# Optimization experiments

Measured on AMD Instinct MI355X. Metric: run time of the kernel, lower is better.

## Reference

```python
import jax, jax.numpy as jnp
import numpy as np

C, PE, L, HEADS = 256, 64, 6, 4
N_GRAPHS, S = 2048, 64            # uniform graphs of S nodes -> dense batch is a reshape
N = N_GRAPHS * S                  # 131072 nodes
E = N * 4                         # 524288 edges
BN_EPS = 1e-5


def _bn(h, g, b):
    # BatchNorm1d, training-mode statistics (biased variance), affine
    m = h.mean(0)
    v = h.var(0)
    return (h - m) / jnp.sqrt(v + BN_EPS) * g + b


def setup_inputs() -> dict:
    key = jax.random.key(0)
    ks = iter(jax.random.split(key, 64))
    def rn(shape, scale=0.05):
        return jax.random.normal(next(ks), shape, dtype=jnp.float32) * scale
    x = jax.random.randint(next(ks), (N, 1), 0, 28)
    pe = jax.random.normal(next(ks), (N, 20), dtype=jnp.float32)
    epg = E // N_GRAPHS
    base = (jnp.arange(E) // epg) * S          # edges stay within their graph
    src = base + jax.random.randint(next(ks), (E,), 0, S)
    dst = base + jax.random.randint(next(ks), (E,), 0, S)
    edge_index = jnp.stack([src, dst])
    edge_attr = jax.random.randint(next(ks), (E,), 0, 4)
    batch = jnp.arange(N) // S
    return dict(
        x=x, pe=pe, edge_index=edge_index, edge_attr=edge_attr, batch=batch,
        node_emb=rn((28, C - PE), 1.0), pe_lin_w=rn((20, PE)), pe_lin_b=jnp.zeros(PE),
        pe_norm_g=jnp.ones(20), pe_norm_b=jnp.zeros(20),
        edge_emb=rn((4, C), 1.0),
        conv_w1=rn((L, C, C)), conv_b1=jnp.zeros((L, C)),
        conv_w2=rn((L, C, C)), conv_b2=jnp.zeros((L, C)),
        attn_in_w=rn((L, C, 3 * C)), attn_in_b=jnp.zeros((L, 3 * C)),
        attn_out_w=rn((L, C, C)), attn_out_b=jnp.zeros((L, C)),
        bn1_g=jnp.ones((L, C)), bn1_b=jnp.zeros((L, C)),
        bn2_g=jnp.ones((L, C)), bn2_b=jnp.zeros((L, C)),
        bn3_g=jnp.ones((L, C)), bn3_b=jnp.zeros((L, C)),
        mlp_w1=rn((L, C, 2 * C)), mlp_b1=jnp.zeros((L, 2 * C)),
        mlp_w2=rn((L, 2 * C, C)), mlp_b2=jnp.zeros((L, C)),
        head_w1=rn((C, C // 2)), head_b1=jnp.zeros(C // 2),
        head_w2=rn((C // 2, C // 4)), head_b2=jnp.zeros(C // 4),
        head_w3=rn((C // 4, 1)), head_b3=jnp.zeros(1),
    )


def reference(x, pe, edge_index, edge_attr, batch, node_emb, pe_lin_w, pe_lin_b,
              pe_norm_g, pe_norm_b, edge_emb, conv_w1, conv_b1, conv_w2, conv_b2,
              attn_in_w, attn_in_b, attn_out_w, attn_out_b,
              bn1_g, bn1_b, bn2_g, bn2_b, bn3_g, bn3_b,
              mlp_w1, mlp_b1, mlp_w2, mlp_b2,
              head_w1, head_b1, head_w2, head_b2, head_w3, head_b3):
    x_pe = _bn(pe, pe_norm_g, pe_norm_b)
    h = jnp.concatenate([node_emb[x[:, 0]], x_pe @ pe_lin_w + pe_lin_b], axis=1)  # [N, C]
    ea = edge_emb[edge_attr]                                                      # [E, C]
    src, dst = edge_index[0], edge_index[1]
    d = C // HEADS
    scale = 1.0 / jnp.sqrt(jnp.float32(d))
    for l in range(L):
        # --- local GINEConv: nn((1+eps)*x_i + sum_j relu(x_j + e_ij)), eps=0 ---
        msg = jax.nn.relu(h[src] + ea)                          # gather + add + relu
        aggr = jax.ops.segment_sum(msg, dst, num_segments=N)    # scatter-add
        z = h + aggr
        hl = jax.nn.relu(z @ conv_w1[l] + conv_b1[l]) @ conv_w2[l] + conv_b2[l]
        hl = _bn(hl + h, bn1_g[l], bn1_b[l])                    # residual + norm1
        # --- global multihead attention on dense batch [G, S, C] ---
        hd = h.reshape(N_GRAPHS, S, C)
        qkv = hd @ attn_in_w[l] + attn_in_b[l]
        q, k, v = jnp.split(qkv, 3, axis=-1)
        q = q.reshape(N_GRAPHS, S, HEADS, d).transpose(0, 2, 1, 3)
        k = k.reshape(N_GRAPHS, S, HEADS, d).transpose(0, 2, 1, 3)
        v = v.reshape(N_GRAPHS, S, HEADS, d).transpose(0, 2, 1, 3)
        a = jax.nn.softmax(jnp.einsum('ghqd,ghkd->ghqk', q, k) * scale, axis=-1)
        o = jnp.einsum('ghqk,ghkd->ghqd', a, v).transpose(0, 2, 1, 3).reshape(N_GRAPHS, S, C)
        o = (o @ attn_out_w[l] + attn_out_b[l]).reshape(N, C)
        ha = _bn(o + h, bn2_g[l], bn2_b[l])                     # residual + norm2
        # --- combine + FFN ---
        out = hl + ha
        ff = jax.nn.relu(out @ mlp_w1[l] + mlp_b1[l]) @ mlp_w2[l] + mlp_b2[l]
        h = _bn(out + ff, bn3_g[l], bn3_b[l])                   # residual + norm3
    pooled = jax.ops.segment_sum(h, batch, num_segments=N_GRAPHS)  # global_add_pool -> [G, C]
    t = jax.nn.relu(pooled @ head_w1 + head_b1)
    t = jax.nn.relu(t @ head_w2 + head_b2)
    return t @ head_w3 + head_b3                                   # [G, 1]
```

## Files before the change

### kernel.cpp

```cpp
#include <hip/hip_runtime.h>

#define N_NODES 131072
#define N_EDGES 524288
#define CCH 256
#define N_GRAPHS_ 2048
#define SEQ 64
#define LAYERS 6

typedef unsigned short US;
typedef __attribute__((ext_vector_type(8))) short v8s;
typedef __attribute__((ext_vector_type(8))) unsigned short v8us;
typedef __attribute__((ext_vector_type(4))) float v4f;

__device__ __forceinline__ float b2f(US u) { return __uint_as_float(((unsigned)u) << 16); }
__device__ __forceinline__ US f2b(float f) {
    unsigned u = __float_as_uint(f);
    return (US)((u + 0x7fff + ((u >> 16) & 1)) >> 16);
}
__device__ __forceinline__ void gload16(const US* g, US* l) {
    __builtin_amdgcn_global_load_lds(
        (const __attribute__((address_space(1))) unsigned int*)g,
        (__attribute__((address_space(3))) unsigned int*)l, 16, 0, 0);
}

__device__ float g_stats[512];
__device__ float g_aff1[512];
__device__ float g_aff2[512];
__device__ float g_aff3[512];
__device__ float g_pe[40];
__device__ float g_peaff[40];
__device__ US    g_wt[6 * 655360];
__device__ int   g_csr[N_EDGES];
__device__ int   g_off[N_GRAPHS_ * 65];

__global__ __launch_bounds__(256) void wt_k(const float* __restrict__ cw1, const float* __restrict__ cw2,
                                            const float* __restrict__ aiw, const float* __restrict__ aow,
                                            const float* __restrict__ mw1, const float* __restrict__ mw2) {
    __shared__ float t[64][65];
    int b = blockIdx.x;
    int l = b / 160, r = b % 160;
    const float* src; int ldw, ldk, ctiles; size_t doff;
    if (r < 16)      { src = cw1 + (size_t)l * 65536;  ldw = 256; ldk = 256; ctiles = 4;  doff = 0;      }
    else if (r < 32) { src = cw2 + (size_t)l * 65536;  ldw = 256; ldk = 256; ctiles = 4;  doff = 65536;  r -= 16; }
    else if (r < 80) { src = aiw + (size_t)l * 196608; ldw = 768; ldk = 256; ctiles = 12; doff = 131072; r -= 32; }
    else if (r < 96) { src = aow + (size_t)l * 65536;  ldw = 256; ldk = 256; ctiles = 4;  doff = 327680; r -= 80; }
    else if (r < 128){ src = mw1 + (size_t)l * 131072; ldw = 512; ldk = 256; ctiles = 8;  doff = 393216; r -= 96; }
    else             { src = mw2 + (size_t)l * 131072; ldw = 256; ldk = 512; ctiles = 4;  doff = 524288; r -= 128; }
    int kt = r / ctiles, ct = r % ctiles;
    int k0 = kt * 64, c0 = ct * 64;
    US* dst = g_wt + (size_t)l * 655360 + doff;
    int tid = threadIdx.x;
    int rr = tid >> 4, c4 = (tid & 15) * 4;
    #pragma unroll
    for (int j = 0; j < 4; j++) {
        float4 v = *(const float4*)(src + (size_t)(k0 + rr + j * 16) * ldw + c0 + c4);
        t[rr + j * 16][c4 + 0] = v.x; t[rr + j * 16][c4 + 1] = v.y;
        t[rr + j * 16][c4 + 2] = v.z; t[rr + j * 16][c4 + 3] = v.w;
    }
    __syncthreads();
    #pragma unroll
    for (int j = 0; j < 4; j++) {
        int crow = rr + j * 16;
        ushort4 o;
        o.x = f2b(t[c4 + 0][crow]); o.y = f2b(t[c4 + 1][crow]);
        o.z = f2b(t[c4 + 2][crow]); o.w = f2b(t[c4 + 3][crow]);
        *(ushort4*)(dst + (size_t)(c0 + crow) * ldk + k0 + c4) = o;
    }
}

__global__ __launch_bounds__(256) void csr_k(const int* __restrict__ ei,
                                             const int* __restrict__ attr) {
    __shared__ int deg[64], off[65];
    int g = blockIdx.x, tid = threadIdx.x;
    if (tid < 64) deg[tid] = 0;
    __syncthreads();
    int e = g * 256 + tid;
    int d = ei[N_EDGES + e] - g * 64;
    int slot = atomicAdd(&deg[d], 1);
    __syncthreads();
    if (tid == 0) {
        off[0] = 0;
        for (int i = 0; i < 64; i++) off[i + 1] = off[i] + deg[i];
    }
    __syncthreads();
    g_csr[g * 256 + off[d] + slot] = (ei[e] - g * 64) | (attr[e] << 6);
    if (tid < 65) g_off[g * 65 + tid] = off[tid];
}

__global__ __launch_bounds__(256) void pe_part_k(const float* __restrict__ pe) {
    __shared__ float red[240], red2[240];
    int b = blockIdx.x, tid = threadIdx.x;
    float s = 0.f, s2 = 0.f;
    if (tid < 240) {
        int ch = tid % 20, sub = tid / 20;
        size_t r0 = (size_t)b * 512;
        for (int r = sub; r < 512; r += 12) {
            float v = pe[(r0 + r) * 20 + ch];
            s += v; s2 += v * v;
        }
        red[tid] = s; red2[tid] = s2;
    }
    __syncthreads();
    if (tid < 20) {
        float ts = 0.f, ts2 = 0.f;
        #pragma unroll
        for (int sub = 0; sub < 12; sub++) { ts += red[sub * 20 + tid]; ts2 += red2[sub * 20 + tid]; }
        atomicAdd(&g_pe[tid], ts);
        atomicAdd(&g_pe[20 + tid], ts2);
    }
}

__global__ __launch_bounds__(64) void pe_fin_k(const float* __restrict__ g,
                                               const float* __restrict__ b) {
    int t = threadIdx.x;
    if (t < 20) {
        float mean = g_pe[t] / (float)N_NODES;
        float var  = g_pe[20 + t] / (float)N_NODES - mean * mean;
        float a = g[t] * rsqrtf(var + 1e-5f);
        g_peaff[t] = a;
        g_peaff[20 + t] = b[t] - mean * a;
        g_pe[t] = 0.f;
        g_pe[20 + t] = 0.f;
    }
}

__global__ __launch_bounds__(256) void embed_k(const int* __restrict__ x,
                                               const float* __restrict__ pe,
                                               const float* __restrict__ node_emb,
                                               const float* __restrict__ plw,
                                               const float* __restrict__ plb,
                                               US* __restrict__ h) {
    int n = blockIdx.x;
    int tid = threadIdx.x;
    int xi = x[n];
    float v;
    if (tid < 192) {
        v = node_emb[xi * 192 + tid];
    } else {
        int j = tid - 192;
        float s = plb[j];
        #pragma unroll
        for (int k = 0; k < 20; k++) {
            float p = pe[(size_t)n * 20 + k] * g_peaff[k] + g_peaff[20 + k];
            s += p * plw[k * 64 + j];
        }
        v = s;
    }
    h[(size_t)n * CCH + tid] = f2b(v);
}

__global__ __launch_bounds__(256) void apply_k(US* __restrict__ h) {
    size_t idx = (size_t)blockIdx.x * 256 + threadIdx.x;
    size_t stride = (size_t)gridDim.x * 256;
    for (; idx < (size_t)N_NODES * CCH / 8; idx += stride) {
        size_t i = idx * 8;
        int c = (int)(i & 255);
        v8us a = *(const v8us*)(h + i);
        v8us o;
        #pragma unroll
        for (int j = 0; j < 8; j++)
            o[j] = f2b(b2f(a[j]) * g_aff3[c + j] + g_aff3[CCH + c + j]);
        *(v8us*)(h + i) = o;
    }
}

__global__ __launch_bounds__(256) void aggr_z_k(const US* __restrict__ h,
                                                const float* __restrict__ eemb,
                                                US* __restrict__ z) {
    __shared__ US ht[64 * 264];
    __shared__ float em[4 * 260];
    __shared__ int off[65], ce[256];
    int g = blockIdx.x, tid = threadIdx.x;
    for (int v = tid; v < 2048; v += 256) {
        int row = v >> 5, seg = (v & 31) * 8;
        *(v8us*)&ht[row * 264 + seg] = *(const v8us*)(h + (size_t)(g * 64 + row) * 256 + seg);
    }
    for (int i = tid; i < 1024; i += 256)
        em[(i >> 8) * 260 + (i & 255)] = eemb[(i >> 8) * 256 + (i & 255)];
    ce[tid] = g_csr[g * 256 + tid];
    if (tid < 65) off[tid] = g_off[g * 65 + tid];
    __syncthreads();

    int dst = tid >> 2, cq = (tid & 3) * 4;
    float acc[64];
    #pragma unroll
    for (int i = 0; i < 64; i++) acc[i] = 0.f;
    int e1 = off[dst + 1];
    for (int e = off[dst]; e < e1; e++) {
        int val = ce[e];
        int src = val & 63, a = (val >> 6) & 3;
        #pragma unroll
        for (int i = 0; i < 16; i++) {
            int c = cq + i * 16;
            ushort4 hv = *(ushort4*)&ht[src * 264 + c];
            float4 ev = *(float4*)&em[a * 260 + c];
            acc[i * 4 + 0] += fmaxf(b2f(hv.x) + ev.x, 0.f);
            acc[i * 4 + 1] += fmaxf(b2f(hv.y) + ev.y, 0.f);
            acc[i * 4 + 2] += fmaxf(b2f(hv.z) + ev.z, 0.f);
            acc[i * 4 + 3] += fmaxf(b2f(hv.w) + ev.w, 0.f);
        }
    }
    US* zp = z + (size_t)(g * 64 + dst) * 256;
    #pragma unroll
    for (int i = 0; i < 16; i++) {
        int c = cq + i * 16;
        ushort4 hv = *(ushort4*)&ht[dst * 264 + c];
        ushort4 o;
        o.x = f2b(b2f(hv.x) + acc[i * 4 + 0]);
        o.y = f2b(b2f(hv.y) + acc[i * 4 + 1]);
        o.z = f2b(b2f(hv.z) + acc[i * 4 + 2]);
        o.w = f2b(b2f(hv.w) + acc[i * 4 + 3]);
        *(ushort4*)(zp + c) = o;
    }
}

template<int NG, bool STATS>
__global__ __launch_bounds__(256, 4) void gemm_mfma_k(const US* __restrict__ A,
                                                      size_t woff, int ldk,
                                                      int w0, int w1, int w2, int w3,
                                                      const float* __restrict__ bias,
                                                      const US* __restrict__ res,
                                                      US* __restrict__ Y, int mode) {
    const US* __restrict__ Wt = g_wt + woff;
    __shared__ __align__(16) char smem[8192 + 2 * NG * 4096];
    US* As0 = (US*)smem;
    US* As1 = As0 + 2048;
    US* Bs0 = (US*)(smem + 8192);
    US* Bs1 = Bs0 + NG * 2048;
    float* Es = (float*)smem;
    const int NW = NG * 64 + 4;

    int tid = threadIdx.x;
    int bid = blockIdx.x;
    int swz = (bid & 7) * ((int)gridDim.x >> 3) + (bid >> 3);
    size_t row0 = (size_t)swz * 64;
    int w = tid >> 6, l = tid & 63;
    int li = l & 15, hi = l >> 4;
    int sl = hi ^ ((li >> 1) & 3);
    int sr = l >> 2, ss = l & 3;

    int a_off = (w * 16 + li) * 32 + sl * 8;

    v4f acc[NG * 4];
    #pragma unroll
    for (int t = 0; t < NG * 4; t++) acc[t] = (v4f){0.f, 0.f, 0.f, 0.f};

    int ar = w * 16 + sr;
    int akg = (ss ^ ((ar >> 1) & 3)) * 8;
    const US* asrc = A + (row0 + ar) * 256 + akg;

    auto stage = [&](int kc, US* Asb, US* Bsb) {
        int k0 = kc * 32;
        gload16(asrc + k0, Asb + w * 512);
        #pragma unroll
        for (int j = 0; j < NG; j++) {
            int cu = (j * 4 + w) * 16 + sr;
            int grp = cu >> 6;
            int wb = (grp == 0) ? w0 : (grp == 1) ? w1 : (grp == 2) ? w2 : w3;
            int kg = (ss ^ ((cu >> 1) & 3)) * 8;
            gload16(Wt + (size_t)(wb + (cu & 63)) * ldk + k0 + kg,
                    Bsb + (j * 4 + w) * 512);
        }
    };

    stage(0, As0, Bs0);
    __syncthreads();
    for (int kc = 0; kc < 8; kc++) {
        US* Asc = (kc & 1) ? As1 : As0;
        US* Bsc = (kc & 1) ? Bs1 : Bs0;
        if (kc < 7) stage(kc + 1, (kc & 1) ? As0 : As1, (kc & 1) ? Bs0 : Bs1);
        v8s a0 = *(v8s*)(Asc + a_off);
        #pragma unroll
        for (int t = 0; t < NG * 4; t++) {
            v8s bf = *(v8s*)(Bsc + (t * 16 + li) * 32 + sl * 8);
            acc[t] = __builtin_amdgcn_mfma_f32_16x16x32_bf16(a0, bf, acc[t], 0, 0, 0);
        }
        __syncthreads();
    }

    int er_f = tid >> 3;
    int lcb = (tid & 7) * 8;
    float csum = 0.f, csum2 = 0.f;
    #pragma unroll
    for (int p = 0; p < 2; p++) {
        if ((w >> 1) == p) {
            int er0 = (w & 1) * 16 + hi * 4;
            #pragma unroll
            for (int t = 0; t < NG * 4; t++) {
                int grp = t >> 2;
                int wb = (grp == 0) ? w0 : (grp == 1) ? w1 : (grp == 2) ? w2 : w3;
                float bv = bias ? bias[wb + (t & 3) * 16 + li] : 0.f;
                #pragma unroll
                for (int r = 0; r < 4; r++) {
                    float v = acc[t][r] + bv;
                    if (mode == 1) v = fmaxf(v, 0.f);
                    Es[(er0 + r) * NW + t * 16 + li] = v;
                }
            }
        }
        __syncthreads();
        size_t gr = row0 + p * 32 + er_f;
        #pragma unroll
        for (int s = 0; s < NG; s++) {
            int c = s * 64 + lcb;
            float vs[8];
            #pragma unroll
            for (int j = 0; j < 8; j++) vs[j] = Es[er_f * NW + c + j];
            if (mode == 2) {
                v8us rv = *(const v8us*)(res + gr * 256 + c);
                #pragma unroll
                for (int j = 0; j < 8; j++) vs[j] += b2f(rv[j]);
            }
            v8us yv;
            #pragma unroll
            for (int j = 0; j < 8; j++) yv[j] = f2b(vs[j]);
            *(v8us*)(Y + gr * 256 + c) = yv;
            if constexpr (STATS) {
                #pragma unroll
                for (int j = 0; j < 8; j++) Es[er_f * NW + c + j] = vs[j];
            }
        }
        if constexpr (STATS) {
            __syncthreads();
            if (tid < NG * 64) {
                float s1 = 0.f, s2 = 0.f;
                #pragma unroll 8
                for (int r2 = 0; r2 < 32; r2++) {
                    float vv = Es[r2 * NW + tid];
                    s1 += vv; s2 += vv * vv;
                }
                csum += s1; csum2 += s2;
            }
        }
        __syncthreads();
    }
    if constexpr (STATS) {
        if (tid < NG * 64) {
            atomicAdd(&g_stats[tid], csum);
            atomicAdd(&g_stats[CCH + tid], csum2);
        }
    }
}

template<int NH>
__global__ __launch_bounds__(256, 2) void mlp_fused_k(const US* __restrict__ A,
                                                      size_t woff1, const float* __restrict__ bias1,
                                                      size_t woff2, int ldk2,
                                                      const float* __restrict__ bias2,
                                                      const US* __restrict__ res,
                                                      US* __restrict__ Y) {
    const US* __restrict__ W1t = g_wt + woff1;
    const US* __restrict__ W2t = g_wt + woff2;
    __shared__ __align__(16) char smem[73728];
    US* As0 = (US*)smem;
    US* As1 = (US*)(smem + 4096);
    US* Bs0 = (US*)(smem + 8192);
    US* Bs1 = (US*)(smem + 24576);
    float* Es = (float*)smem;
    US* Ts = (US*)(smem + 40960);

    int tid = threadIdx.x;
    int bid = blockIdx.x;
    int swz = (bid & 7) * ((int)gridDim.x >> 3) + (bid >> 3);
    size_t row0 = (size_t)swz * 64;
    int w = tid >> 6, l = tid & 63;
    int li = l & 15, hi = l >> 4;
    int sl = hi ^ ((li >> 1) & 3);
    int sr = l >> 2, ss = l & 3;

    int a_off = (w * 16 + li) * 32 + sl * 8;

    v4f accY[16];
    #pragma unroll
    for (int t = 0; t < 16; t++) accY[t] = (v4f){0.f, 0.f, 0.f, 0.f};

    int ar = w * 16 + sr;
    int akg = (ss ^ ((ar >> 1) & 3)) * 8;
    const US* asrc = A + (row0 + ar) * 256 + akg;

    #pragma unroll
    for (int q = 0; q < NH; q++) {
        v4f accT[16];
        #pragma unroll
        for (int t = 0; t < 16; t++) accT[t] = (v4f){0.f, 0.f, 0.f, 0.f};

        auto stageA = [&](int kc, US* Asb, US* Bsb) {
            int k0 = kc * 32;
            gload16(asrc + k0, Asb + w * 512);
            #pragma unroll
            for (int j = 0; j < 4; j++) {
                int cu = (j * 4 + w) * 16 + sr;
                int kg = (ss ^ ((cu >> 1) & 3)) * 8;
                gload16(W1t + (size_t)(q * 256 + cu) * 256 + k0 + kg,
                        Bsb + (j * 4 + w) * 512);
            }
        };
        stageA(0, As0, Bs0);
        __syncthreads();
        for (int kc = 0; kc < 8; kc++) {
            US* Asc = (kc & 1) ? As1 : As0;
            US* Bsc = (kc & 1) ? Bs1 : Bs0;
            if (kc < 7) stageA(kc + 1, (kc & 1) ? As0 : As1, (kc & 1) ? Bs0 : Bs1);
            v8s a0 = *(v8s*)(Asc + a_off);
            #pragma unroll
            for (int t = 0; t < 16; t++) {
                v8s bf = *(v8s*)(Bsc + (t * 16 + li) * 32 + sl * 8);
                accT[t] = __builtin_amdgcn_mfma_f32_16x16x32_bf16(a0, bf, accT[t], 0, 0, 0);
            }
            __syncthreads();
        }
        #pragma unroll
        for (int p = 0; p < 2; p++) {
            if ((w >> 1) == p) {
                int er0 = (w & 1) * 16 + hi * 4;
                #pragma unroll
                for (int t = 0; t < 16; t++) {
                    float bv = bias1[q * 256 + t * 16 + li];
                    #pragma unroll
                    for (int r = 0; r < 4; r++)
                        Es[(er0 + r) * 260 + t * 16 + li] = fmaxf(accT[t][r] + bv, 0.f);
                }
            }
            __syncthreads();
            {
                int er = tid >> 3, lcb = (tid & 7) * 8;
                int rowL = p * 32 + er;
                int rsw = (rowL >> 1) & 3;
                #pragma unroll
                for (int s = 0; s < 4; s++) {
                    int col = s * 64 + lcb;
                    v8us tv;
                    #pragma unroll
                    for (int j = 0; j < 8; j++) tv[j] = f2b(Es[er * 260 + col + j]);
                    int chunk = col >> 5, slot = ((col >> 3) & 3) ^ rsw;
                    *(v8us*)&Ts[chunk * 2048 + rowL * 32 + slot * 8] = tv;
                }
            }
            __syncthreads();
        }
        auto stageB = [&](int kc, US* Bsb) {
            int k0 = q * 256 + kc * 32;
            #pragma unroll
            for (int j = 0; j < 4; j++) {
                int cu = (j * 4 + w) * 16 + sr;
                int kg = (ss ^ ((cu >> 1) & 3)) * 8;
                gload16(W2t + (size_t)cu * ldk2 + k0 + kg, Bsb + (j * 4 + w) * 512);
            }
        };
        stageB(0, Bs0);
        __syncthreads();
        for (int kc = 0; kc < 8; kc++) {
            US* Bsc = (kc & 1) ? Bs1 : Bs0;
            if (kc < 7) stageB(kc + 1, (kc & 1) ? Bs0 : Bs1);
            v8s a0 = *(v8s*)(Ts + kc * 2048 + a_off);
            #pragma unroll
            for (int t = 0; t < 16; t++) {
                v8s bf = *(v8s*)(Bsc + (t * 16 + li) * 32 + sl * 8);
                accY[t] = __builtin_amdgcn_mfma_f32_16x16x32_bf16(a0, bf, accY[t], 0, 0, 0);
            }
            __syncthreads();
        }
    }

    int er_f = tid >> 3;
    int lcb = (tid & 7) * 8;
    float csum = 0.f, csum2 = 0.f;
    #pragma unroll
    for (int p = 0; p < 2; p++) {
        if ((w >> 1) == p) {
            int er0 = (w & 1) * 16 + hi * 4;
            #pragma unroll
            for (int t = 0; t < 16; t++) {
                float bv = bias2[t * 16 + li];
                #pragma unroll
                for (int r = 0; r < 4; r++)
                    Es[(er0 + r) * 260 + t * 16 + li] = accY[t][r] + bv;
            }
        }
        __syncthreads();
        size_t gr = row0 + p * 32 + er_f;
        #pragma unroll
        for (int s = 0; s < 4; s++) {
            int c = s * 64 + lcb;
            float vs[8];
            #pragma unroll
            for (int j = 0; j < 8; j++) vs[j] = Es[er_f * 260 + c + j];
            v8us rv = *(const v8us*)(res + gr * 256 + c);
            #pragma unroll
            for (int j = 0; j < 8; j++) vs[j] += b2f(rv[j]);
            v8us yv;
            #pragma unroll
            for (int j = 0; j < 8; j++) yv[j] = f2b(vs[j]);
            *(v8us*)(Y + gr * 256 + c) = yv;
            #pragma unroll
            for (int j = 0; j < 8; j++) Es[er_f * 260 + c + j] = vs[j];
        }
        __syncthreads();
        {
            float s1 = 0.f, s2 = 0.f;
            #pragma unroll 8
            for (int r2 = 0; r2 < 32; r2++) {
                float vv = Es[r2 * 260 + tid];
                s1 += vv; s2 += vv * vv;
            }
            csum += s1; csum2 += s2;
        }
        __syncthreads();
    }
    atomicAdd(&g_stats[tid], csum);
    atomicAdd(&g_stats[CCH + tid], csum2);
}

__global__ __launch_bounds__(64) void attn_k(US* __restrict__ qb,
                                             const US* __restrict__ kb,
                                             const US* __restrict__ vb) {
    __shared__ __align__(16) US Ps[64 * 72];
    __shared__ __align__(16) US Vt[64 * 72];
    int g = blockIdx.x, l = threadIdx.x;
    int coff = blockIdx.y * 64;
    int li = l & 15, hi8 = (l >> 4) * 8, hi4 = (l >> 4) * 4;
    size_t rb = (size_t)g * 64 * 256;

    {
        v8us vv[8];
        #pragma unroll
        for (int jv = 0; jv < 8; jv++)
            vv[jv] = *(const v8us*)(vb + rb + l * 256 + coff + jv * 8);
        #pragma unroll
        for (int jv = 0; jv < 8; jv++)
            #pragma unroll
            for (int e = 0; e < 8; e++)
                Vt[(jv * 8 + e) * 72 + l] = vv[jv][e];
    }

    v8s Qf[4][2], Kf[4][2];
    #pragma unroll
    for (int t = 0; t < 4; t++)
        #pragma unroll
        for (int ds = 0; ds < 2; ds++) {
            Qf[t][ds] = *(const v8s*)(qb + rb + (t * 16 + li) * 256 + coff + ds * 32 + hi8);
            Kf[t][ds] = *(const v8s*)(kb + rb + (t * 16 + li) * 256 + coff + ds * 32 + hi8);
        }

    v4f S[4][4];
    #pragma unroll
    for (int qt = 0; qt < 4; qt++)
        #pragma unroll
        for (int kt = 0; kt < 4; kt++) {
            v4f a = (v4f){0.f, 0.f, 0.f, 0.f};
            a = __builtin_amdgcn_mfma_f32_16x16x32_bf16(Qf[qt][0], Kf[kt][0], a, 0, 0, 0);
            a = __builtin_amdgcn_mfma_f32_16x16x32_bf16(Qf[qt][1], Kf[kt][1], a, 0, 0, 0);
            S[qt][kt] = a;
        }

    #pragma unroll
    for (int qt = 0; qt < 4; qt++)
        #pragma unroll
        for (int r = 0; r < 4; r++) {
            float mx = -1e30f;
            #pragma unroll
            for (int kt = 0; kt < 4; kt++) {
                S[qt][kt][r] *= 0.125f;
                mx = fmaxf(mx, S[qt][kt][r]);
            }
            mx = fmaxf(mx, __shfl_xor(mx, 1));
            mx = fmaxf(mx, __shfl_xor(mx, 2));
            mx = fmaxf(mx, __shfl_xor(mx, 4));
            mx = fmaxf(mx, __shfl_xor(mx, 8));
            float sum = 0.f;
            #pragma unroll
            for (int kt = 0; kt < 4; kt++) {
                float e = __expf(S[qt][kt][r] - mx);
                S[qt][kt][r] = e;
                sum += e;
            }
            sum += __shfl_xor(sum, 1);
            sum += __shfl_xor(sum, 2);
            sum += __shfl_xor(sum, 4);
            sum += __shfl_xor(sum, 8);
            float inv = 1.f / sum;
            #pragma unroll
            for (int kt = 0; kt < 4; kt++)
                Ps[(qt * 16 + hi4 + r) * 72 + kt * 16 + li] = f2b(S[qt][kt][r] * inv);
        }

    v4f O[4][4];
    #pragma unroll
    for (int qt = 0; qt < 4; qt++)
        #pragma unroll
        for (int jt = 0; jt < 4; jt++) O[qt][jt] = (v4f){0.f, 0.f, 0.f, 0.f};
    #pragma unroll
    for (int ks = 0; ks < 2; ks++) {
        v8s Pf[4], Vf[4];
        #pragma unroll
        for (int qt = 0; qt < 4; qt++)
            Pf[qt] = *(v8s*)&Ps[(qt * 16 + li) * 72 + ks * 32 + hi8];
        #pragma unroll
        for (int jt = 0; jt < 4; jt++)
            Vf[jt] = *(v8s*)&Vt[(jt * 16 + li) * 72 + ks * 32 + hi8];
        #pragma unroll
        for (int qt = 0; qt < 4; qt++)
            #pragma unroll
            for (int jt = 0; jt < 4; jt++)
                O[qt][jt] = __builtin_amdgcn_mfma_f32_16x16x32_bf16(Pf[qt], Vf[jt], O[qt][jt], 0, 0, 0);
    }

    __syncthreads();
    #pragma unroll
    for (int qt = 0; qt < 4; qt++)
        #pragma unroll
        for (int jt = 0; jt < 4; jt++)
            #pragma unroll
            for (int r = 0; r < 4; r++)
                Ps[(qt * 16 + hi4 + r) * 72 + jt * 16 + li] = f2b(O[qt][jt][r]);
    __syncthreads();
    US* ob = qb + rb + l * 256 + coff;
    #pragma unroll
    for (int jv = 0; jv < 8; jv++)
        *(v8us*)(ob + jv * 8) = *(v8us*)&Ps[l * 72 + jv * 8];
}

__global__ __launch_bounds__(256) void affine_k(const float* __restrict__ g,
                                                const float* __restrict__ b, int sel) {
    int c = threadIdx.x;
    float mean = g_stats[c] / (float)N_NODES;
    float var  = g_stats[CCH + c] / (float)N_NODES - mean * mean;
    float a = g[c] * rsqrtf(var + 1e-5f);
    float* dst = (sel == 0) ? g_aff1 : (sel == 1) ? g_aff2 : g_aff3;
    dst[c] = a;
    dst[CCH + c] = b[c] - mean * a;
    g_stats[c] = 0.f;
    g_stats[CCH + c] = 0.f;
}

__global__ __launch_bounds__(256) void combine_k(const US* __restrict__ y1,
                                                 const US* __restrict__ y2,
                                                 US* __restrict__ out) {
    size_t idx = (size_t)blockIdx.x * 256 + threadIdx.x;
    size_t stride = (size_t)gridDim.x * 256;
    for (; idx < (size_t)N_NODES * CCH / 8; idx += stride) {
        size_t i = idx * 8;
        int c = (int)(i & 255);
        v8us a = *(const v8us*)(y1 + i);
        v8us b = *(const v8us*)(y2 + i);
        v8us o;
        #pragma unroll
        for (int j = 0; j < 8; j++) {
            float v = b2f(a[j]) * g_aff1[c + j] + g_aff1[CCH + c + j] +
                      b2f(b[j]) * g_aff2[c + j] + g_aff2[CCH + c + j];
            o[j] = f2b(v);
        }
        *(v8us*)(out + i) = o;
    }
}

__global__ __launch_bounds__(256) void pool_k(const US* __restrict__ h,
                                              float* __restrict__ pooled) {
    int g = blockIdx.x, c = threadIdx.x;
    float s = 0.f;
    for (int ss = 0; ss < SEQ; ss++) s += b2f(h[((size_t)g * SEQ + ss) * CCH + c]);
    pooled[(size_t)g * CCH + c] = g_aff3[c] * s + 64.f * g_aff3[CCH + c];
}

__global__ __launch_bounds__(128) void head_k(const float* __restrict__ pooled,
                                              const float* __restrict__ w1, const float* __restrict__ b1,
                                              const float* __restrict__ w2, const float* __restrict__ b2,
                                              const float* __restrict__ w3, const float* __restrict__ b3,
                                              float* __restrict__ outp) {
    __shared__ float p[256], t1[128], t2[64];
    int g = blockIdx.x, tid = threadIdx.x;
    p[tid] = pooled[(size_t)g * CCH + tid];
    p[tid + 128] = pooled[(size_t)g * CCH + 128 + tid];
    __syncthreads();
    float s = b1[tid];
    for (int k = 0; k < 256; k++) s += p[k] * w1[k * 128 + tid];
    t1[tid] = fmaxf(s, 0.f);
    __syncthreads();
    if (tid < 64) {
        float s2 = b2[tid];
        for (int k = 0; k < 128; k++) s2 += t1[k] * w2[k * 64 + tid];
        t2[tid] = fmaxf(s2, 0.f);
    }
    __syncthreads();
    if (tid == 0) {
        float s3 = b3[0];
        for (int k = 0; k < 64; k++) s3 += t2[k] * w3[k];
        outp[g] = s3;
    }
}

extern "C" void kernel_launch(void* const* d_in, const int* in_sizes, int n_in,
                              void* d_out, int out_size, void* d_ws, size_t ws_size,
                              hipStream_t stream) {
    const int*   x         = (const int*)  d_in[0];
    const float* pe        = (const float*)d_in[1];
    const int*   ei        = (const int*)  d_in[2];
    const int*   eattr     = (const int*)  d_in[3];
    const float* node_emb  = (const float*)d_in[5];
    const float* pe_lin_w  = (const float*)d_in[6];
    const float* pe_lin_b  = (const float*)d_in[7];
    const float* pe_norm_g = (const float*)d_in[8];
    const float* pe_norm_b = (const float*)d_in[9];
    const float* edge_emb  = (const float*)d_in[10];
    const float* conv_w1   = (const float*)d_in[11];
    const float* conv_b1   = (const float*)d_in[12];
    const float* conv_w2   = (const float*)d_in[13];
    const float* conv_b2   = (const float*)d_in[14];
    const float* attn_in_w = (const float*)d_in[15];
    const float* attn_in_b = (const float*)d_in[16];
    const float* attn_out_w= (const float*)d_in[17];
    const float* attn_out_b= (const float*)d_in[18];
    const float* bn1_g     = (const float*)d_in[19];
    const float* bn1_b     = (const float*)d_in[20];
    const float* bn2_g     = (const float*)d_in[21];
    const float* bn2_b     = (const float*)d_in[22];
    const float* bn3_g     = (const float*)d_in[23];
    const float* bn3_b     = (const float*)d_in[24];
    const float* mlp_w1    = (const float*)d_in[25];
    const float* mlp_b1    = (const float*)d_in[26];
    const float* mlp_w2    = (const float*)d_in[27];
    const float* mlp_b2    = (const float*)d_in[28];
    const float* head_w1   = (const float*)d_in[29];
    const float* head_b1   = (const float*)d_in[30];
    const float* head_w2   = (const float*)d_in[31];
    const float* head_b2   = (const float*)d_in[32];
    const float* head_w3   = (const float*)d_in[33];
    const float* head_b3   = (const float*)d_in[34];
    (void)in_sizes; (void)n_in; (void)out_size; (void)ws_size;

    char* ws = (char*)d_ws;
    US* h = (US*)(ws);
    US* A = (US*)(ws + 67108864ULL);
    US* B = (US*)(ws + 134217728ULL);
    US* C = (US*)(ws + 201326592ULL);
    float* pooled = (float*)(ws + 67108864ULL);

    wt_k<<<960, 256, 0, stream>>>(conv_w1, conv_w2, attn_in_w, attn_out_w, mlp_w1, mlp_w2);
    csr_k<<<N_GRAPHS_, 256, 0, stream>>>(ei, eattr);
    pe_part_k<<<256, 256, 0, stream>>>(pe);
    pe_fin_k<<<1, 64, 0, stream>>>(pe_norm_g, pe_norm_b);
    embed_k<<<N_NODES, 256, 0, stream>>>(x, pe, node_emb, pe_lin_w, pe_lin_b, h);

    for (int l = 0; l < LAYERS; l++) {
        size_t wl = (size_t)l * 655360;

        if (l > 0) apply_k<<<2048, 256, 0, stream>>>(h);

        gemm_mfma_k<4, false><<<2048, 256, 0, stream>>>(h, wl + 131072, 256, 0, 64, 128, 192,
                                                        attn_in_b + l * 768, nullptr, A, 0);
        gemm_mfma_k<4, false><<<2048, 256, 0, stream>>>(h, wl + 131072, 256, 256, 320, 384, 448,
                                                        attn_in_b + l * 768, nullptr, B, 0);
        gemm_mfma_k<4, false><<<2048, 256, 0, stream>>>(h, wl + 131072, 256, 512, 576, 640, 704,
                                                        attn_in_b + l * 768, nullptr, C, 0);
        attn_k<<<dim3(N_GRAPHS_, 4), 64, 0, stream>>>(A, B, C);
        gemm_mfma_k<4, true><<<2048, 256, 0, stream>>>(A, wl + 327680, 256, 0, 64, 128, 192,
                                                       attn_out_b + l * 256, h, B, 2);
        affine_k<<<1, 256, 0, stream>>>(bn2_g + l * 256, bn2_b + l * 256, 1);

        aggr_z_k<<<N_GRAPHS_, 256, 0, stream>>>(h, edge_emb, C);
        mlp_fused_k<1><<<2048, 256, 0, stream>>>(C, wl, conv_b1 + l * 256,
                                                 wl + 65536, 256, conv_b2 + l * 256,
                                                 h, C);
        affine_k<<<1, 256, 0, stream>>>(bn1_g + l * 256, bn1_b + l * 256, 0);

        combine_k<<<2048, 256, 0, stream>>>(C, B, A);
        mlp_fused_k<2><<<2048, 256, 0, stream>>>(A, wl + 393216, mlp_b1 + l * 512,
                                                 wl + 524288, 512, mlp_b2 + l * 256,
                                                 A, h);
        affine_k<<<1, 256, 0, stream>>>(bn3_g + l * 256, bn3_b + l * 256, 2);
    }

    pool_k<<<N_GRAPHS_, 256, 0, stream>>>(h, pooled);
    head_k<<<N_GRAPHS_, 128, 0, stream>>>(pooled, head_w1, head_b1, head_w2, head_b2,
                                          head_w3, head_b3, (float*)d_out);
}
```

Measured before the change: 5.023 ms.

## Fuse the three QKV projection GEMMs into one kernel reusing the staged input tile

Replaces the three separate Q/K/V GEMM launches with a single qkv_k kernel. Each block stages its 64x256 slice of h in LDS once and loops over three output projections, streaming the weight tiles with double buffering. This removes two of the three reads of the activation matrix per layer and two kernel launches. In exchange it uses more shared memory per block, and the epilogue scratch overlaps the weight buffers, so the next projection's first weight tile is prefetched and then restaged a second time.

```diff
diff --git a/kernel.cpp b/kernel.cpp
--- a/kernel.cpp
+++ b/kernel.cpp
@@ -338,6 +338,104 @@
         if (tid < NG * 64) {
             atomicAdd(&g_stats[tid], csum);
             atomicAdd(&g_stats[CCH + tid], csum2);
+        }
+    }
+}
+
+__global__ __launch_bounds__(256, 2) void qkv_k(const US* __restrict__ h,
+                                                size_t woff,
+                                                const float* __restrict__ bias,
+                                                US* __restrict__ Q, US* __restrict__ K,
+                                                US* __restrict__ V) {
+    const US* __restrict__ Wt = g_wt + woff;
+    __shared__ __align__(16) char smem[66560];
+    US* AsP = (US*)smem;
+    US* Bs0 = (US*)(smem + 32768);
+    US* Bs1 = (US*)(smem + 49152);
+    float* Es = (float*)(smem + 32768);
+    const int NW = 260;
+
+    int tid = threadIdx.x;
+    int bid = blockIdx.x;
+    int swz = (bid & 7) * ((int)gridDim.x >> 3) + (bid >> 3);
+    size_t row0 = (size_t)swz * 64;
+    int w = tid >> 6, l = tid & 63;
+    int li = l & 15, hi = l >> 4;
+    int sl = hi ^ ((li >> 1) & 3);
+    int sr = l >> 2, ss = l & 3;
+
+    int a_off = (w * 16 + li) * 32 + sl * 8;
+
+    int ar = w * 16 + sr;
+    int akg = (ss ^ ((ar >> 1) & 3)) * 8;
+    const US* asrc = h + (row0 + ar) * 256 + akg;
+
+    #pragma unroll
+    for (int kc = 0; kc < 8; kc++)
+        gload16(asrc + kc * 32, AsP + kc * 2048 + w * 512);
+
+    auto stageB = [&](int out, int kc, US* Bsb) {
+        int k0 = kc * 32;
+        #pragma unroll
+        for (int j = 0; j < 4; j++) {
+            int cu = (j * 4 + w) * 16 + sr;
+            int kg = (ss ^ ((cu >> 1) & 3)) * 8;
+            gload16(Wt + (size_t)(out * 256 + cu) * 256 + k0 + kg,
+                    Bsb + (j * 4 + w) * 512);
+        }
+    };
+
+    stageB(0, 0, Bs0);
+    __syncthreads();
+
+    #pragma unroll
+    for (int out = 0; out < 3; out++) {
+        v4f acc[16];
+        #pragma unroll
+        for (int t = 0; t < 16; t++) acc[t] = (v4f){0.f, 0.f, 0.f, 0.f};
+
+        for (int kc = 0; kc < 8; kc++) {
+            US* Bsc = (kc & 1) ? Bs1 : Bs0;
+            if (kc < 7)      stageB(out, kc + 1, (kc & 1) ? Bs0 : Bs1);
+            else if (out < 2) stageB(out + 1, 0, (kc & 1) ? Bs0 : Bs1);
+            v8s a0 = *(v8s*)(AsP + kc * 2048 + a_off);
+            #pragma unroll
+            for (int t = 0; t < 16; t++) {
+                v8s bf = *(v8s*)(Bsc + (t * 16 + li) * 32 + sl * 8);
+                acc[t] = __builtin_amdgcn_mfma_f32_16x16x32_bf16(a0, bf, acc[t], 0, 0, 0);
+            }
+            __syncthreads();
+        }
+
+        US* Y = (out == 0) ? Q : (out == 1) ? K : V;
+        #pragma unroll
+        for (int p = 0; p < 2; p++) {
+            if ((w >> 1) == p) {
+                int er0 = (w & 1) * 16 + hi * 4;
+                #pragma unroll
+                for (int t = 0; t < 16; t++) {
+                    float bv = bias[out * 256 + t * 16 + li];
+                    #pragma unroll
+                    for (int r = 0; r < 4; r++)
+                        Es[(er0 + r) * NW + t * 16 + li] = acc[t][r] + bv;
+                }
+            }
+            __syncthreads();
+            size_t gr = row0 + p * 32 + (tid >> 3);
+            int lcb = (tid & 7) * 8;
+            #pragma unroll
+            for (int s = 0; s < 4; s++) {
+                int c = s * 64 + lcb;
+                v8us yv;
+                #pragma unroll
+                for (int j = 0; j < 8; j++) yv[j] = f2b(Es[(tid >> 3) * NW + c + j]);
+                *(v8us*)(Y + gr * 256 + c) = yv;
+            }
+            __syncthreads();
+        }
+        if (out < 2) {
+            stageB(out + 1, 0, Bs0);
+            __syncthreads();
         }
     }
 }
@@ -746,12 +844,7 @@
 
         if (l > 0) apply_k<<<2048, 256, 0, stream>>>(h);
 
-        gemm_mfma_k<4, false><<<2048, 256, 0, stream>>>(h, wl + 131072, 256, 0, 64, 128, 192,
-                                                        attn_in_b + l * 768, nullptr, A, 0);
-        gemm_mfma_k<4, false><<<2048, 256, 0, stream>>>(h, wl + 131072, 256, 256, 320, 384, 448,
-                                                        attn_in_b + l * 768, nullptr, B, 0);
-        gemm_mfma_k<4, false><<<2048, 256, 0, stream>>>(h, wl + 131072, 256, 512, 576, 640, 704,
-                                                        attn_in_b + l * 768, nullptr, C, 0);
+        qkv_k<<<2048, 256, 0, stream>>>(h, wl + 131072, attn_in_b + l * 768, A, B, C);
         attn_k<<<dim3(N_GRAPHS_, 4), 64, 0, stream>>>(A, B, C);
         gemm_mfma_k<4, true><<<2048, 256, 0, stream>>>(A, wl + 327680, 256, 0, 64, 128, 192,
                                                        attn_out_b + l * 256, h, B, 2);
```

New measurement: 5.240 ms. 1.04x slower.
